# Optimization experiments

Hardware: AMD Instinct MI355X
Metric: run time of the kernel (lower is better)

The kernel has to match this reference:

```python
import jax, jax.numpy as jnp
import numpy as np

SCALING = 2.0  # lora_alpha / r


def setup_inputs() -> dict:
    key = jax.random.key(0)
    ks = jax.random.split(key, 6)
    B, S, D_IN, D_OUT, R = 4, 4096, 4096, 4096, 32
    x = jax.random.normal(ks[0], (B, S, D_IN), dtype=jnp.float32)
    W = jax.random.normal(ks[1], (D_OUT, D_IN), dtype=jnp.float32) * 0.02
    b = jax.random.normal(ks[2], (D_OUT,), dtype=jnp.float32) * 0.02
    A = jax.random.normal(ks[3], (R, D_IN), dtype=jnp.float32) * 0.02
    B_w = jax.random.normal(ks[4], (D_OUT, R), dtype=jnp.float32) * 0.02
    # per-sample activation offsets, in [1, S]
    alora_offsets = jax.random.randint(ks[5], (B,), 1, S + 1, dtype=jnp.int32)
    return {"x": x, "alora_offsets": alora_offsets, "W": W, "b": b, "A": A, "B_w": B_w}


def reference(x, alora_offsets, W, b, A, B_w):
    # base linear: y = x @ W^T + b
    base = jnp.einsum("bsd,od->bso", x, W) + b  # [B, S, D_OUT]
    # LoRA path on full sequence (dropout is identity at inference, p=0)
    lora = jnp.einsum("bsr,or->bso", jnp.einsum("bsd,rd->bsr", x, A), B_w) * SCALING
    # per-sample tail mask: only last k = min(offset, S) positions get the LoRA update
    S = x.shape[1]
    k = jnp.minimum(alora_offsets, S)  # [B]
    pos = jnp.arange(S, dtype=jnp.int32)
    mask = pos[None, :] >= (S - k)[:, None]  # [B, S] True on the tail
    return base + jnp.where(mask[:, :, None], lora, jnp.zeros((), base.dtype))
```

## Files before the change

kernel.cpp:

```cpp
#include <hip/hip_runtime.h>
#include <hip/hip_bf16.h>

typedef __attribute__((ext_vector_type(8))) short short8;
typedef __attribute__((ext_vector_type(4))) float f32x4;

#define GLOAD_LDS16(gp, lp)                                                      \
  __builtin_amdgcn_global_load_lds(                                              \
      (const __attribute__((address_space(1))) void*)(gp),                       \
      (__attribute__((address_space(3))) void*)(lp), 16, 0, 0)

#define SBAR() asm volatile("s_barrier" ::: "memory")
#define VMC(n)                                                                   \
  do {                                                                           \
    asm volatile("s_waitcnt vmcnt(" #n ")" ::: "memory");                        \
    __builtin_amdgcn_sched_barrier(0);                                           \
  } while (0)

__device__ __forceinline__ unsigned short f2bf_rne(float f) {
  union { float f; unsigned int u; } v; v.f = f;
  unsigned int u = v.u;
  u += 0x7fffu + ((u >> 16) & 1u);
  return (unsigned short)(u >> 16);
}

__device__ __forceinline__ short8 pack8(f32x4 a, f32x4 b) {
  short8 o;
  o[0] = (short)f2bf_rne(a[0]); o[1] = (short)f2bf_rne(a[1]);
  o[2] = (short)f2bf_rne(a[2]); o[3] = (short)f2bf_rne(a[3]);
  o[4] = (short)f2bf_rne(b[0]); o[5] = (short)f2bf_rne(b[1]);
  o[6] = (short)f2bf_rne(b[2]); o[7] = (short)f2bf_rne(b[3]);
  return o;
}

__global__ void cvt_f32_bf16(const float* __restrict__ src,
                             unsigned short* __restrict__ dst, int n8) {
  int i = blockIdx.x * blockDim.x + threadIdx.x;
  int stride = gridDim.x * blockDim.x;
  const f32x4* s4 = (const f32x4*)src;
  short8* d8 = (short8*)dst;
  for (; i < n8; i += stride) {
    d8[i] = pack8(s4[2 * i], s4[2 * i + 1]);
  }
}

__global__ __launch_bounds__(256) void cvt_lora_kernel(
    const float* __restrict__ x,
    const float* __restrict__ A,
    const float* __restrict__ W,
    const int* __restrict__ offs,
    unsigned short* __restrict__ xb,
    unsigned short* __restrict__ Wb,
    unsigned short* __restrict__ T)
{
  __shared__ unsigned short xs[32 * 72];
  __shared__ unsigned short as_[32 * 72];
  const int t = threadIdx.x;
  const int m0 = blockIdx.x * 32;
  const int l = t & 63, w = t >> 6;
  const int wr = w >> 1, wc = w & 1;
  const int lr = l & 15, lk = (l >> 4) * 8;
  const int arow = t >> 3, acol = (t & 7) * 8;
  f32x4 acc = {0, 0, 0, 0};
  for (int kt = 0; kt < 64; ++kt) {
    const int kof = kt * 64 + acol;
    const float* px = x + (size_t)(m0 + arow) * 4096 + kof;
    const float* pa = A + (size_t)arow * 4096 + kof;
    short8 s0 = pack8(*(const f32x4*)px, *(const f32x4*)(px + 4));
    short8 sa = pack8(*(const f32x4*)pa, *(const f32x4*)(pa + 4));
    *(short8*)(xb + (size_t)(m0 + arow) * 4096 + kof) = s0;
    __syncthreads();
    *(short8*)&xs[arow * 72 + acol]  = s0;
    *(short8*)&as_[arow * 72 + acol] = sa;
    __syncthreads();
#pragma unroll
    for (int kk = 0; kk < 2; ++kk) {
      short8 a = *(const short8*)&xs[(wr * 16 + lr) * 72 + kk * 32 + lk];
      short8 b = *(const short8*)&as_[(wc * 16 + lr) * 72 + kk * 32 + lk];
      acc = __builtin_amdgcn_mfma_f32_16x16x32_bf16(a, b, acc, 0, 0, 0);
    }
  }
  const int rowb = (l >> 4) * 4;
#pragma unroll
  for (int j = 0; j < 4; ++j) {
    int m = m0 + wr * 16 + rowb + j;
    int bb = m >> 12, s = m & 4095;
    int kcut = offs[bb]; if (kcut > 4096) kcut = 4096;
    bool keep = s >= 4096 - kcut;
    T[(size_t)m * 32 + wc * 16 + lr] = keep ? f2bf_rne(2.0f * acc[j]) : (unsigned short)0;
  }
  const f32x4* s4 = (const f32x4*)W;
  short8* d8 = (short8*)Wb;
  const int base = blockIdx.x * 4096;
#pragma unroll
  for (int q = 0; q < 16; ++q) {
    int idx = base + q * 256 + t;
    d8[idx] = pack8(s4[2 * idx], s4[2 * idx + 1]);
  }
}

__global__ __launch_bounds__(512, 2) void gemm_kernel(
    const unsigned short* __restrict__ xb,
    const unsigned short* __restrict__ Wb,
    const unsigned short* __restrict__ Tm,
    const unsigned short* __restrict__ Bwb,
    const float* __restrict__ bias,
    float* __restrict__ out)
{
  constexpr int K = 4096;
  extern __shared__ char smem[];

  const int bid = blockIdx.x;
  const int swz = (bid & 7) * 128 + (bid >> 3);
  const int m0 = (swz >> 4) * 256;
  const int n0 = (swz & 15) * 256;

  const int t = threadIdx.x;
  const int l = t & 63, w = t >> 6;
  const int wqr = w >> 2;
  const int pr = (w >> 1) & 1;
  const int pc = w & 1;
  const int lr = l & 15, hi = l >> 4;
  const int e0 = (hi ^ (lr & 7)) * 8;

  const int srow = t >> 3;
  const int schunk = ((t & 7) ^ ((t >> 3) & 7)) * 8;
  const unsigned short* pA0 = xb + (size_t)(m0 + srow) * K + schunk;
  const unsigned short* pA1 = xb + (size_t)(m0 + 128 + srow) * K + schunk;
  const unsigned short* pB0 = Wb + (size_t)(n0 + srow) * K + schunk;
  const unsigned short* pB1 = Wb + (size_t)(n0 + 128 + srow) * K + schunk;
  unsigned short* sm = (unsigned short*)smem;
  const int ldst = t * 16;

#define STG(PTR, SLOT, ISB, HALF, KT)                                           \
  do {                                                                          \
    const unsigned short* g_ = (PTR) + (KT) * 64;                               \
    char* d_ = smem + (SLOT) * 65536 + (ISB) * 32768 + (HALF) * 16384 + ldst;   \
    GLOAD_LDS16(g_, d_);                                                        \
    GLOAD_LDS16(g_ + (size_t)64 * K, d_ + 8192);                                \
  } while (0)

  f32x4 acc[2][4][4];
  short8 afr[4];

  {
    const unsigned short* tp = Tm + (size_t)(m0 + wqr * 128 + pr * 64 + lr) * 32 + hi * 8;
    short8 la[4];
#pragma unroll
    for (int i = 0; i < 4; ++i) la[i] = *(const short8*)(tp + i * 512);
    short8 lb[2][4];
#pragma unroll
    for (int qc = 0; qc < 2; ++qc)
#pragma unroll
      for (int j = 0; j < 4; ++j)
        lb[qc][j] = *(const short8*)(Bwb + (size_t)(n0 + qc * 128 + pc * 64 + j * 16 + lr) * 32 + hi * 8);
#pragma unroll
    for (int qc = 0; qc < 2; ++qc)
#pragma unroll
      for (int i = 0; i < 4; ++i)
#pragma unroll
        for (int j = 0; j < 4; ++j)
          acc[qc][i][j] = __builtin_amdgcn_mfma_f32_16x16x32_bf16(
              la[i], lb[qc][j], (f32x4){0.f, 0.f, 0.f, 0.f}, 0, 0, 0);
  }

  STG(pB1, 0, 1, 1, 0);
  STG(pA0, 0, 0, 0, 0);
  STG(pA1, 0, 0, 1, 0);
  STG(pB0, 0, 1, 0, 0);
  STG(pB0, 1, 1, 0, 1);
  VMC(2);
  SBAR();

#define PHASE(SLOT, QC, KK, READA, STG_STMT, WAIT_STMT)                         \
  {                                                                             \
    const unsigned short* Ah = sm + (SLOT) * 32768 + wqr * 8192;                \
    const unsigned short* Bh = sm + (SLOT) * 32768 + 16384 + (QC) * 8192;       \
    const int ek = e0 ^ ((KK) * 32);                                            \
    if (READA) {                                                                \
      _Pragma("unroll")                                                         \
      for (int i = 0; i < 4; ++i)                                               \
        afr[i] = *(const short8*)(Ah + (pr * 64 + i * 16 + lr) * 64 + ek);      \
    }                                                                           \
    short8 bfr[4];                                                              \
    _Pragma("unroll")                                                           \
    for (int j = 0; j < 4; ++j)                                                 \
      bfr[j] = *(const short8*)(Bh + (pc * 64 + j * 16 + lr) * 64 + ek);        \
    STG_STMT;                                                                   \
    SBAR();                                                                     \
    __builtin_amdgcn_s_setprio(1);                                              \
    _Pragma("unroll")                                                           \
    for (int i = 0; i < 4; ++i)                                                 \
      _Pragma("unroll")                                                         \
      for (int j = 0; j < 4; ++j)                                               \
        acc[QC][i][j] = __builtin_amdgcn_mfma_f32_16x16x32_bf16(                \
            afr[i], bfr[j], acc[QC][i][j], 0, 0, 0);                            \
    __builtin_amdgcn_s_setprio(0);                                              \
    WAIT_STMT;                                                                  \
    SBAR();                                                                     \
  }

  for (int I = 0; I < 31; ++I) {
    const int a = 2 * I;
    PHASE(0, 0, 0, 1, STG(pB1, 1, 1, 1, a + 1), ((void)0));
    PHASE(0, 1, 0, 0, STG(pA0, 1, 0, 0, a + 1), ((void)0));
    PHASE(0, 0, 1, 1, STG(pA1, 1, 0, 1, a + 1), ((void)0));
    PHASE(0, 1, 1, 0, STG(pB0, 0, 1, 0, a + 2), VMC(2));
    PHASE(1, 0, 0, 1, STG(pB1, 0, 1, 1, a + 2), ((void)0));
    PHASE(1, 1, 0, 0, STG(pA0, 0, 0, 0, a + 2), ((void)0));
    PHASE(1, 0, 1, 1, STG(pA1, 0, 0, 1, a + 2), ((void)0));
    PHASE(1, 1, 1, 0, STG(pB0, 1, 1, 0, a + 3), VMC(2));
  }
  PHASE(0, 0, 0, 1, STG(pB1, 1, 1, 1, 63), ((void)0));
  PHASE(0, 1, 0, 0, STG(pA0, 1, 0, 0, 63), ((void)0));
  PHASE(0, 0, 1, 1, STG(pA1, 1, 0, 1, 63), ((void)0));
  PHASE(0, 1, 1, 0, ((void)0), VMC(0));
  PHASE(1, 0, 0, 1, ((void)0), ((void)0));
  PHASE(1, 1, 0, 0, ((void)0), ((void)0));
  PHASE(1, 0, 1, 1, ((void)0), ((void)0));
  PHASE(1, 1, 1, 0, ((void)0), ((void)0));
#undef PHASE
#undef STG

  float bv[2][4];
#pragma unroll
  for (int qc = 0; qc < 2; ++qc)
#pragma unroll
    for (int j = 0; j < 4; ++j)
      bv[qc][j] = bias[n0 + qc * 128 + pc * 64 + j * 16 + lr];
  const int rowb = hi * 4;
#pragma unroll
  for (int qc = 0; qc < 2; ++qc)
#pragma unroll
    for (int i = 0; i < 4; ++i)
#pragma unroll
      for (int e = 0; e < 4; ++e) {
        int row = m0 + wqr * 128 + pr * 64 + i * 16 + rowb + e;
        float* orow = out + (size_t)row * 4096 + n0 + qc * 128 + pc * 64;
#pragma unroll
        for (int j = 0; j < 4; ++j) orow[j * 16 + lr] = acc[qc][i][j][e] + bv[qc][j];
      }
}

extern "C" void kernel_launch(void* const* d_in, const int* in_sizes, int n_in,
                              void* d_out, int out_size, void* d_ws, size_t ws_size,
                              hipStream_t stream) {
  const float* x   = (const float*)d_in[0];
  const int* offs  = (const int*)d_in[1];
  const float* W   = (const float*)d_in[2];
  const float* b   = (const float*)d_in[3];
  const float* A   = (const float*)d_in[4];
  const float* Bw  = (const float*)d_in[5];
  float* out = (float*)d_out;

  char* ws = (char*)d_ws;
  unsigned short* xb  = (unsigned short*)ws;
  unsigned short* Wb  = (unsigned short*)(ws + 134217728);
  unsigned short* Bwb = (unsigned short*)(ws + 167772160);
  unsigned short* T   = (unsigned short*)(ws + 168034304);

  hipFuncSetAttribute((const void*)gemm_kernel,
                      hipFuncAttributeMaxDynamicSharedMemorySize, 131072);

  cvt_f32_bf16<<<64, 256, 0, stream>>>(Bw, Bwb, 131072 / 8);
  cvt_lora_kernel<<<512, 256, 0, stream>>>(x, A, W, offs, xb, Wb, T);
  gemm_kernel<<<1024, 512, 131072, stream>>>(xb, Wb, T, Bwb, b, out);
}
```

Baseline: 581.4 us.

## Ping-pong warp groups between LDS reads and MFMA phases

Splits the eight waves into two groups that alternate roles each barrier step: one group issues LDS fragment reads and global-to-LDS prefetches while the other runs its MFMA block. The goal is to overlap LDS and memory traffic with matrix compute across waves instead of having all waves read and then compute in lockstep. This doubles the barrier count and relies on the existing wait/slot schedule staying race-free with the staggered groups, which raises correctness and scheduling risk.

New measurement: 616.2 us. 1.06x slower.

```diff
diff --git a/kernel.cpp b/kernel.cpp
--- a/kernel.cpp
+++ b/kernel.cpp
@@ -117,6 +117,7 @@
   const int t = threadIdx.x;
   const int l = t & 63, w = t >> 6;
   const int wqr = w >> 2;
+  const bool tA = (wqr == 0);
   const int pr = (w >> 1) & 1;
   const int pc = w & 1;
   const int lr = l & 15, hi = l >> 4;
@@ -140,7 +141,7 @@
   } while (0)
 
   f32x4 acc[2][4][4];
-  short8 afr[4];
+  short8 afr[4], bfr[4];
 
   {
     const unsigned short* tp = Tm + (size_t)(m0 + wqr * 128 + pr * 64 + lr) * 32 + hi * 8;
@@ -162,6 +163,37 @@
           acc[qc][i][j] = __builtin_amdgcn_mfma_f32_16x16x32_bf16(
               la[i], lb[qc][j], (f32x4){0.f, 0.f, 0.f, 0.f}, 0, 0, 0);
   }
+
+#define RD(SLOT, QC, KK, READA, STG_STMT, WAIT_STMT)                            \
+  do {                                                                          \
+    const unsigned short* Ah = sm + (SLOT) * 32768 + wqr * 8192;                \
+    const unsigned short* Bh = sm + (SLOT) * 32768 + 16384 + (QC) * 8192;       \
+    const int ek = e0 ^ ((KK) * 32);                                            \
+    if (READA) {                                                                \
+      _Pragma("unroll")                                                         \
+      for (int i_ = 0; i_ < 4; ++i_)                                            \
+        afr[i_] = *(const short8*)(Ah + (pr * 64 + i_ * 16 + lr) * 64 + ek);    \
+    }                                                                           \
+    _Pragma("unroll")                                                           \
+    for (int j_ = 0; j_ < 4; ++j_)                                              \
+      bfr[j_] = *(const short8*)(Bh + (pc * 64 + j_ * 16 + lr) * 64 + ek);      \
+    STG_STMT;                                                                   \
+    WAIT_STMT;                                                                  \
+  } while (0)
+
+#define MM(QC)                                                                  \
+  do {                                                                          \
+    __builtin_amdgcn_s_setprio(1);                                              \
+    _Pragma("unroll")                                                           \
+    for (int i_ = 0; i_ < 4; ++i_)                                              \
+      _Pragma("unroll")                                                         \
+      for (int j_ = 0; j_ < 4; ++j_)                                            \
+        acc[QC][i_][j_] = __builtin_amdgcn_mfma_f32_16x16x32_bf16(              \
+            afr[i_], bfr[j_], acc[QC][i_][j_], 0, 0, 0);                        \
+    __builtin_amdgcn_s_setprio(0);                                              \
+  } while (0)
+
+#define NOP ((void)0)
 
   STG(pB1, 0, 1, 1, 0);
   STG(pA0, 0, 0, 0, 0);
@@ -171,54 +203,47 @@
   VMC(2);
   SBAR();
 
-#define PHASE(SLOT, QC, KK, READA, STG_STMT, WAIT_STMT)                         \
-  {                                                                             \
-    const unsigned short* Ah = sm + (SLOT) * 32768 + wqr * 8192;                \
-    const unsigned short* Bh = sm + (SLOT) * 32768 + 16384 + (QC) * 8192;       \
-    const int ek = e0 ^ ((KK) * 32);                                            \
-    if (READA) {                                                                \
-      _Pragma("unroll")                                                         \
-      for (int i = 0; i < 4; ++i)                                               \
-        afr[i] = *(const short8*)(Ah + (pr * 64 + i * 16 + lr) * 64 + ek);      \
-    }                                                                           \
-    short8 bfr[4];                                                              \
-    _Pragma("unroll")                                                           \
-    for (int j = 0; j < 4; ++j)                                                 \
-      bfr[j] = *(const short8*)(Bh + (pc * 64 + j * 16 + lr) * 64 + ek);        \
-    STG_STMT;                                                                   \
-    SBAR();                                                                     \
-    __builtin_amdgcn_s_setprio(1);                                              \
-    _Pragma("unroll")                                                           \
-    for (int i = 0; i < 4; ++i)                                                 \
-      _Pragma("unroll")                                                         \
-      for (int j = 0; j < 4; ++j)                                               \
-        acc[QC][i][j] = __builtin_amdgcn_mfma_f32_16x16x32_bf16(                \
-            afr[i], bfr[j], acc[QC][i][j], 0, 0, 0);                            \
-    __builtin_amdgcn_s_setprio(0);                                              \
-    WAIT_STMT;                                                                  \
-    SBAR();                                                                     \
-  }
+  if (tA) RD(0, 0, 0, 1, STG(pB1, 1, 1, 1, 1), NOP);
+  SBAR();
 
   for (int I = 0; I < 31; ++I) {
     const int a = 2 * I;
-    PHASE(0, 0, 0, 1, STG(pB1, 1, 1, 1, a + 1), ((void)0));
-    PHASE(0, 1, 0, 0, STG(pA0, 1, 0, 0, a + 1), ((void)0));
-    PHASE(0, 0, 1, 1, STG(pA1, 1, 0, 1, a + 1), ((void)0));
-    PHASE(0, 1, 1, 0, STG(pB0, 0, 1, 0, a + 2), VMC(2));
-    PHASE(1, 0, 0, 1, STG(pB1, 0, 1, 1, a + 2), ((void)0));
-    PHASE(1, 1, 0, 0, STG(pA0, 0, 0, 0, a + 2), ((void)0));
-    PHASE(1, 0, 1, 1, STG(pA1, 0, 0, 1, a + 2), ((void)0));
-    PHASE(1, 1, 1, 0, STG(pB0, 1, 1, 0, a + 3), VMC(2));
-  }
-  PHASE(0, 0, 0, 1, STG(pB1, 1, 1, 1, 63), ((void)0));
-  PHASE(0, 1, 0, 0, STG(pA0, 1, 0, 0, 63), ((void)0));
-  PHASE(0, 0, 1, 1, STG(pA1, 1, 0, 1, 63), ((void)0));
-  PHASE(0, 1, 1, 0, ((void)0), VMC(0));
-  PHASE(1, 0, 0, 1, ((void)0), ((void)0));
-  PHASE(1, 1, 0, 0, ((void)0), ((void)0));
-  PHASE(1, 0, 1, 1, ((void)0), ((void)0));
-  PHASE(1, 1, 1, 0, ((void)0), ((void)0));
-#undef PHASE
+    if (tA) MM(0); else RD(0, 0, 0, 1, STG(pB1, 1, 1, 1, a + 1), NOP);  SBAR();
+    if (tA) RD(0, 1, 0, 0, STG(pA0, 1, 0, 0, a + 1), NOP); else MM(0); SBAR();
+    if (tA) MM(1); else RD(0, 1, 0, 0, STG(pA0, 1, 0, 0, a + 1), NOP);  SBAR();
+    if (tA) RD(0, 0, 1, 1, STG(pA1, 1, 0, 1, a + 1), NOP); else MM(1); SBAR();
+    if (tA) MM(0); else RD(0, 0, 1, 1, STG(pA1, 1, 0, 1, a + 1), NOP);  SBAR();
+    if (tA) RD(0, 1, 1, 0, STG(pB0, 0, 1, 0, a + 2), VMC(2)); else MM(0); SBAR();
+    if (tA) MM(1); else RD(0, 1, 1, 0, STG(pB0, 0, 1, 0, a + 2), VMC(2)); SBAR();
+    if (tA) RD(1, 0, 0, 1, STG(pB1, 0, 1, 1, a + 2), NOP); else MM(1); SBAR();
+    if (tA) MM(0); else RD(1, 0, 0, 1, STG(pB1, 0, 1, 1, a + 2), NOP);  SBAR();
+    if (tA) RD(1, 1, 0, 0, STG(pA0, 0, 0, 0, a + 2), NOP); else MM(0); SBAR();
+    if (tA) MM(1); else RD(1, 1, 0, 0, STG(pA0, 0, 0, 0, a + 2), NOP);  SBAR();
+    if (tA) RD(1, 0, 1, 1, STG(pA1, 0, 0, 1, a + 2), NOP); else MM(1); SBAR();
+    if (tA) MM(0); else RD(1, 0, 1, 1, STG(pA1, 0, 0, 1, a + 2), NOP);  SBAR();
+    if (tA) RD(1, 1, 1, 0, STG(pB0, 1, 1, 0, a + 3), VMC(2)); else MM(0); SBAR();
+    if (tA) MM(1); else RD(1, 1, 1, 0, STG(pB0, 1, 1, 0, a + 3), VMC(2)); SBAR();
+    if (tA) RD(0, 0, 0, 1, STG(pB1, 1, 1, 1, a + 3), NOP); else MM(1); SBAR();
+  }
+  if (tA) MM(0); else RD(0, 0, 0, 1, STG(pB1, 1, 1, 1, 63), NOP);  SBAR();
+  if (tA) RD(0, 1, 0, 0, STG(pA0, 1, 0, 0, 63), NOP); else MM(0); SBAR();
+  if (tA) MM(1); else RD(0, 1, 0, 0, STG(pA0, 1, 0, 0, 63), NOP);  SBAR();
+  if (tA) RD(0, 0, 1, 1, STG(pA1, 1, 0, 1, 63), NOP); else MM(1); SBAR();
+  if (tA) MM(0); else RD(0, 0, 1, 1, STG(pA1, 1, 0, 1, 63), NOP);  SBAR();
+  if (tA) RD(0, 1, 1, 0, NOP, VMC(0)); else MM(0); SBAR();
+  if (tA) MM(1); else RD(0, 1, 1, 0, NOP, VMC(0));  SBAR();
+  if (tA) RD(1, 0, 0, 1, NOP, NOP); else MM(1); SBAR();
+  if (tA) MM(0); else RD(1, 0, 0, 1, NOP, NOP);  SBAR();
+  if (tA) RD(1, 1, 0, 0, NOP, NOP); else MM(0); SBAR();
+  if (tA) MM(1); else RD(1, 1, 0, 0, NOP, NOP);  SBAR();
+  if (tA) RD(1, 0, 1, 1, NOP, NOP); else MM(1); SBAR();
+  if (tA) MM(0); else RD(1, 0, 1, 1, NOP, NOP);  SBAR();
+  if (tA) RD(1, 1, 1, 0, NOP, NOP); else MM(0); SBAR();
+  if (tA) MM(1); else RD(1, 1, 1, 0, NOP, NOP);  SBAR();
+  if (!tA) MM(1);
+#undef RD
+#undef MM
+#undef NOP
 #undef STG
 
   float bv[2][4];
```

## Load GEMM A operand directly from global into registers, bypassing LDS

Applied to the files above, without the earlier changes.

The x (A) tile is no longer staged through shared memory. Each wave now issues its own inline-asm global_load_dwordx4 into double-buffered register banks, and only the W tile still goes global-to-LDS. This halves the dynamic LDS to 64 KB and removes the A-side LDS reads. The cost is that waves sharing the same A rows fetch them redundantly from global/L2, register pressure rises, and correctness depends on manual vmcnt waits covering the asm loads.

Result: slower. 810.4 us (+39.4%).

```diff
diff --git a/kernel.cpp b/kernel.cpp
--- a/kernel.cpp
+++ b/kernel.cpp
@@ -124,23 +124,44 @@
 
   const int srow = t >> 3;
   const int schunk = ((t & 7) ^ ((t >> 3) & 7)) * 8;
-  const unsigned short* pA0 = xb + (size_t)(m0 + srow) * K + schunk;
-  const unsigned short* pA1 = xb + (size_t)(m0 + 128 + srow) * K + schunk;
   const unsigned short* pB0 = Wb + (size_t)(n0 + srow) * K + schunk;
   const unsigned short* pB1 = Wb + (size_t)(n0 + 128 + srow) * K + schunk;
   unsigned short* sm = (unsigned short*)smem;
   const int ldst = t * 16;
 
-#define STG(PTR, SLOT, ISB, HALF, KT)                                           \
+#define STGB(PTR, SLOT, HALF, KT)                                               \
   do {                                                                          \
     const unsigned short* g_ = (PTR) + (KT) * 64;                               \
-    char* d_ = smem + (SLOT) * 65536 + (ISB) * 32768 + (HALF) * 16384 + ldst;   \
+    char* d_ = smem + (SLOT) * 32768 + (HALF) * 16384 + ldst;                   \
     GLOAD_LDS16(g_, d_);                                                        \
     GLOAD_LDS16(g_ + (size_t)64 * K, d_ + 8192);                                \
   } while (0)
 
+  unsigned long long aad[4];
+#pragma unroll
+  for (int f = 0; f < 4; ++f)
+    aad[f] = (unsigned long long)(xb + (size_t)(m0 + wqr * 128 + pr * 64 + f * 16 + lr) * 4096 + hi * 8);
+
+  short8 ar[2][2][4];
+
+#define LDA_K0(BANK)                                                            \
+  do {                                                                          \
+    asm volatile("global_load_dwordx4 %0, %1, off"            : "=v"(ar[BANK][0][0]) : "v"(aad[0])); \
+    asm volatile("global_load_dwordx4 %0, %1, off"            : "=v"(ar[BANK][0][1]) : "v"(aad[1])); \
+    asm volatile("global_load_dwordx4 %0, %1, off"            : "=v"(ar[BANK][0][2]) : "v"(aad[2])); \
+    asm volatile("global_load_dwordx4 %0, %1, off"            : "=v"(ar[BANK][0][3]) : "v"(aad[3])); \
+  } while (0)
+#define LDA_K1(BANK)                                                            \
+  do {                                                                          \
+    asm volatile("global_load_dwordx4 %0, %1, off offset:64"  : "=v"(ar[BANK][1][0]) : "v"(aad[0])); \
+    asm volatile("global_load_dwordx4 %0, %1, off offset:64"  : "=v"(ar[BANK][1][1]) : "v"(aad[1])); \
+    asm volatile("global_load_dwordx4 %0, %1, off offset:64"  : "=v"(ar[BANK][1][2]) : "v"(aad[2])); \
+    asm volatile("global_load_dwordx4 %0, %1, off offset:64"  : "=v"(ar[BANK][1][3]) : "v"(aad[3])); \
+  } while (0)
+#define ADV()                                                                   \
+  do { aad[0] += 128; aad[1] += 128; aad[2] += 128; aad[3] += 128; } while (0)
+
   f32x4 acc[2][4][4];
-  short8 afr[4];
 
   {
     const unsigned short* tp = Tm + (size_t)(m0 + wqr * 128 + pr * 64 + lr) * 32 + hi * 8;
@@ -163,63 +184,62 @@
               la[i], lb[qc][j], (f32x4){0.f, 0.f, 0.f, 0.f}, 0, 0, 0);
   }
 
-  STG(pB1, 0, 1, 1, 0);
-  STG(pA0, 0, 0, 0, 0);
-  STG(pA1, 0, 0, 1, 0);
-  STG(pB0, 0, 1, 0, 0);
-  STG(pB0, 1, 1, 0, 1);
+  LDA_K0(0); LDA_K1(0); ADV();
+  STGB(pB1, 0, 1, 0);
+  STGB(pB0, 0, 0, 0);
+  STGB(pB0, 1, 0, 1);
   VMC(2);
   SBAR();
 
-#define PHASE(SLOT, QC, KK, READA, STG_STMT, WAIT_STMT)                         \
+#define PHASE(SLOT, QC, KK, BANK, ISSUE_STMT, WAIT_STMT)                        \
   {                                                                             \
-    const unsigned short* Ah = sm + (SLOT) * 32768 + wqr * 8192;                \
-    const unsigned short* Bh = sm + (SLOT) * 32768 + 16384 + (QC) * 8192;       \
+    const unsigned short* Bh = sm + (SLOT) * 16384 + (QC) * 8192;               \
     const int ek = e0 ^ ((KK) * 32);                                            \
-    if (READA) {                                                                \
-      _Pragma("unroll")                                                         \
-      for (int i = 0; i < 4; ++i)                                               \
-        afr[i] = *(const short8*)(Ah + (pr * 64 + i * 16 + lr) * 64 + ek);      \
-    }                                                                           \
     short8 bfr[4];                                                              \
     _Pragma("unroll")                                                           \
-    for (int j = 0; j < 4; ++j)                                                 \
-      bfr[j] = *(const short8*)(Bh + (pc * 64 + j * 16 + lr) * 64 + ek);        \
-    STG_STMT;                                                                   \
+    for (int j_ = 0; j_ < 4; ++j_)                                              \
+      bfr[j_] = *(const short8*)(Bh + (pc * 64 + j_ * 16 + lr) * 64 + ek);      \
+    ISSUE_STMT;                                                                 \
     SBAR();                                                                     \
     __builtin_amdgcn_s_setprio(1);                                              \
     _Pragma("unroll")                                                           \
-    for (int i = 0; i < 4; ++i)                                                 \
+    for (int i_ = 0; i_ < 4; ++i_)                                              \
       _Pragma("unroll")                                                         \
-      for (int j = 0; j < 4; ++j)                                               \
-        acc[QC][i][j] = __builtin_amdgcn_mfma_f32_16x16x32_bf16(                \
-            afr[i], bfr[j], acc[QC][i][j], 0, 0, 0);                            \
+      for (int j_ = 0; j_ < 4; ++j_)                                            \
+        acc[QC][i_][j_] = __builtin_amdgcn_mfma_f32_16x16x32_bf16(              \
+            ar[BANK][KK][i_], bfr[j_], acc[QC][i_][j_], 0, 0, 0);               \
     __builtin_amdgcn_s_setprio(0);                                              \
     WAIT_STMT;                                                                  \
     SBAR();                                                                     \
   }
 
+#define NOP ((void)0)
+
   for (int I = 0; I < 31; ++I) {
     const int a = 2 * I;
-    PHASE(0, 0, 0, 1, STG(pB1, 1, 1, 1, a + 1), ((void)0));
-    PHASE(0, 1, 0, 0, STG(pA0, 1, 0, 0, a + 1), ((void)0));
-    PHASE(0, 0, 1, 1, STG(pA1, 1, 0, 1, a + 1), ((void)0));
-    PHASE(0, 1, 1, 0, STG(pB0, 0, 1, 0, a + 2), VMC(2));
-    PHASE(1, 0, 0, 1, STG(pB1, 0, 1, 1, a + 2), ((void)0));
-    PHASE(1, 1, 0, 0, STG(pA0, 0, 0, 0, a + 2), ((void)0));
-    PHASE(1, 0, 1, 1, STG(pA1, 0, 0, 1, a + 2), ((void)0));
-    PHASE(1, 1, 1, 0, STG(pB0, 1, 1, 0, a + 3), VMC(2));
-  }
-  PHASE(0, 0, 0, 1, STG(pB1, 1, 1, 1, 63), ((void)0));
-  PHASE(0, 1, 0, 0, STG(pA0, 1, 0, 0, 63), ((void)0));
-  PHASE(0, 0, 1, 1, STG(pA1, 1, 0, 1, 63), ((void)0));
-  PHASE(0, 1, 1, 0, ((void)0), VMC(0));
-  PHASE(1, 0, 0, 1, ((void)0), ((void)0));
-  PHASE(1, 1, 0, 0, ((void)0), ((void)0));
-  PHASE(1, 0, 1, 1, ((void)0), ((void)0));
-  PHASE(1, 1, 1, 0, ((void)0), ((void)0));
+    PHASE(0, 0, 0, 0, LDA_K0(1), NOP);
+    PHASE(0, 1, 0, 0, { LDA_K1(1); ADV(); }, NOP);
+    PHASE(0, 0, 1, 0, STGB(pB1, 1, 1, a + 1), NOP);
+    PHASE(0, 1, 1, 0, STGB(pB0, 0, 0, a + 2), VMC(2));
+    PHASE(1, 0, 0, 1, LDA_K0(0), NOP);
+    PHASE(1, 1, 0, 1, { LDA_K1(0); ADV(); }, NOP);
+    PHASE(1, 0, 1, 1, STGB(pB1, 0, 1, a + 2), NOP);
+    PHASE(1, 1, 1, 1, STGB(pB0, 1, 0, a + 3), VMC(2));
+  }
+  PHASE(0, 0, 0, 0, LDA_K0(1), NOP);
+  PHASE(0, 1, 0, 0, LDA_K1(1), NOP);
+  PHASE(0, 0, 1, 0, STGB(pB1, 1, 1, 63), NOP);
+  PHASE(0, 1, 1, 0, NOP, VMC(0));
+  PHASE(1, 0, 0, 1, NOP, NOP);
+  PHASE(1, 1, 0, 1, NOP, NOP);
+  PHASE(1, 0, 1, 1, NOP, NOP);
+  PHASE(1, 1, 1, 1, NOP, NOP);
 #undef PHASE
-#undef STG
+#undef NOP
+#undef STGB
+#undef LDA_K0
+#undef LDA_K1
+#undef ADV
 
   float bv[2][4];
 #pragma unroll
@@ -259,9 +279,9 @@
   unsigned short* T   = (unsigned short*)(ws + 168034304);
 
   hipFuncSetAttribute((const void*)gemm_kernel,
-                      hipFuncAttributeMaxDynamicSharedMemorySize, 131072);
+                      hipFuncAttributeMaxDynamicSharedMemorySize, 65536);
 
   cvt_f32_bf16<<<64, 256, 0, stream>>>(Bw, Bwb, 131072 / 8);
   cvt_lora_kernel<<<512, 256, 0, stream>>>(x, A, W, offs, xb, Wb, T);
-  gemm_kernel<<<1024, 512, 131072, stream>>>(xb, Wb, T, Bwb, b, out);
-}
+  gemm_kernel<<<1024, 512, 65536, stream>>>(xb, Wb, T, Bwb, b, out);
+}
```
